# Kernel optimization log

Hardware: AMD Instinct MI355X
Metric: run time of the kernel (lower is better)

Reference implementation:

```python
import jax, jax.numpy as jnp
import numpy as np
from jax import lax

B, T, D = 1, 2048, 2048
H, KVH, HD = 16, 4, 128
BETA = 0.9
ROPE_BASE = 10000.0


def _causal_prefix_ema(x, beta):
    # x: (B, T, D); m_t = beta * m_{t-1} + (1 - beta) * x_t, m_{-1} = 0
    def step(m, xt):
        m = beta * m + (1.0 - beta) * xt
        return m, m
    _, ys = lax.scan(step, jnp.zeros_like(x[:, 0]), jnp.swapaxes(x, 0, 1))
    return jnp.swapaxes(ys, 0, 1)


def _rotate_half(x):
    x1, x2 = jnp.split(x, 2, axis=-1)
    return jnp.concatenate([-x2, x1], axis=-1)


def _rope_cos_sin(t, hd, dtype):
    inv_freq = 1.0 / (ROPE_BASE ** (jnp.arange(0, hd, 2, dtype=jnp.float32) / hd))
    freqs = jnp.arange(t, dtype=jnp.float32)[:, None] * inv_freq[None, :]  # (T, HD/2)
    emb = jnp.concatenate([freqs, freqs], axis=-1)  # (T, HD)
    return jnp.cos(emb).astype(dtype)[None, None], jnp.sin(emb).astype(dtype)[None, None]


def setup_inputs() -> dict:
    key = jax.random.key(0)
    ks = jax.random.split(key, 8)
    std = 0.02
    return {
        "hidden_states": jax.random.normal(ks[0], (B, T, D), jnp.float32),
        "Wq": jax.random.normal(ks[1], (D, H * HD), jnp.float32) * std,
        "Wk": jax.random.normal(ks[2], (D, KVH * HD), jnp.float32) * std,
        "Wv": jax.random.normal(ks[3], (D, KVH * HD), jnp.float32) * std,
        "Wo": jax.random.normal(ks[4], (H * HD, D), jnp.float32) * std,
        "Wr1": jax.random.normal(ks[5], (D, D // 2), jnp.float32) * std,
        "br1": jnp.zeros((D // 2,), jnp.float32),
        "Wr2": jax.random.normal(ks[6], (D // 2, 2), jnp.float32) * std,
        "br2": jnp.zeros((2,), jnp.float32),
    }


def reference(hidden_states, Wq, Wk, Wv, Wo, Wr1, br1, Wr2, br2):
    b, t, d = hidden_states.shape
    q = hidden_states @ Wq  # (B, T, H*HD)

    # multi-level memories: l1 = raw, l2 = causal prefix EMA
    l2 = _causal_prefix_ema(hidden_states, BETA)

    # router MLP on q + softmax over levels
    h = jax.nn.silu(q @ Wr1 + br1)
    lam = jax.nn.softmax(h @ Wr2 + br2, axis=-1)  # (B, T, 2)
    fused = lam[..., 0:1] * hidden_states + lam[..., 1:2] * l2

    # shape to heads
    q_s = q.reshape(b, t, H, HD).transpose(0, 2, 1, 3)                 # (B, H, T, HD)
    k_s = (fused @ Wk).reshape(b, t, KVH, HD).transpose(0, 2, 1, 3)    # (B, KVH, T, HD)
    v_s = (fused @ Wv).reshape(b, t, KVH, HD).transpose(0, 2, 1, 3)

    # RoPE
    cos, sin = _rope_cos_sin(t, HD, q_s.dtype)
    q_s = q_s * cos + _rotate_half(q_s) * sin
    k_s = k_s * cos + _rotate_half(k_s) * sin

    # repeat kv for GQA
    n_rep = H // KVH
    k_s = jnp.repeat(k_s, n_rep, axis=1)
    v_s = jnp.repeat(v_s, n_rep, axis=1)

    # causal SDPA
    scale = 1.0 / jnp.sqrt(jnp.asarray(HD, q_s.dtype))
    scores = jnp.einsum("bhqd,bhkd->bhqk", q_s, k_s) * scale
    causal = jnp.tril(jnp.ones((t, t), dtype=bool))
    scores = jnp.where(causal[None, None], scores, jnp.finfo(scores.dtype).min)
    attn = jax.nn.softmax(scores, axis=-1)
    out = jnp.einsum("bhqk,bhkd->bhqd", attn, v_s)  # (B, H, T, HD)

    out = out.transpose(0, 2, 1, 3).reshape(b, t, H * HD)
    return out @ Wo
```

## Files before the change

### kernel.cpp

```cpp
#include <hip/hip_runtime.h>
#include <hip/hip_bf16.h>

#define T_SEQ 2048
#define D_MODEL 2048
#define NH 16
#define NKVH 4
#define HD 128

typedef __attribute__((ext_vector_type(8))) short bf16x8;
typedef __attribute__((ext_vector_type(4))) float f32x4;

static __device__ __forceinline__ short f32_to_bf16(float f) {
    unsigned u = __float_as_uint(f);
    u += 0x7fffu + ((u >> 16) & 1u);
    return (short)(u >> 16);
}
static __device__ __forceinline__ float bf16_to_f32(short s) {
    return __uint_as_float(((unsigned)(unsigned short)s) << 16);
}
static __device__ __forceinline__ void gl_to_lds16(const void* g, void* l) {
    __builtin_amdgcn_global_load_lds(
        (const __attribute__((address_space(1))) unsigned int*)g,
        (__attribute__((address_space(3))) unsigned int*)l, 16, 0, 0);
}

template<int BN>
__global__ __launch_bounds__(256, 2) void gemm_bt_kernel(
    const short* __restrict__ A, const short* __restrict__ Bt,
    float* __restrict__ Cf, short* __restrict__ Cb,
    int M, int N, int K, const float* __restrict__ bias, int act)
{
    constexpr int NI = BN / 64;
    constexpr int BCH = BN / 32;
    __shared__ short Alds[2][64 * 64];
    __shared__ short Blds[2][BN * 64];

    const int tid = threadIdx.x;
    const int wave = tid >> 6, lane = tid & 63;
    const int l16 = lane & 15, quad = lane >> 4;
    const int wn = wave * (BN / 4);
    const int m0 = blockIdx.y * 64, n0 = blockIdx.x * BN;
    const int niter = K >> 6;

    f32x4 acc[4][NI] = {};

    #pragma unroll
    for (int p = 0; p < 2; ++p) {
        int li = p * 256 + tid;
        int row = li >> 3, sc = li & 7;
        gl_to_lds16(A + (size_t)(m0 + row) * K + ((sc ^ (row & 7)) * 8),
                    &Alds[0][(size_t)(p * 256 + wave * 64) * 8]);
    }
    #pragma unroll
    for (int p = 0; p < BCH; ++p) {
        int li = p * 256 + tid;
        int row = li >> 3, sc = li & 7;
        gl_to_lds16(Bt + (size_t)(n0 + row) * K + ((sc ^ (row & 7)) * 8),
                    &Blds[0][(size_t)(p * 256 + wave * 64) * 8]);
    }

    for (int t = 0; t < niter; ++t) {
        asm volatile("s_waitcnt vmcnt(0)\n\ts_barrier" ::: "memory");

        if (t + 1 < niter) {
            int k1 = (t + 1) << 6;
            int nb = (t + 1) & 1;
            #pragma unroll
            for (int p = 0; p < 2; ++p) {
                int li = p * 256 + tid;
                int row = li >> 3, sc = li & 7;
                gl_to_lds16(A + (size_t)(m0 + row) * K + k1 + ((sc ^ (row & 7)) * 8),
                            &Alds[nb][(size_t)(p * 256 + wave * 64) * 8]);
            }
            #pragma unroll
            for (int p = 0; p < BCH; ++p) {
                int li = p * 256 + tid;
                int row = li >> 3, sc = li & 7;
                gl_to_lds16(Bt + (size_t)(n0 + row) * K + k1 + ((sc ^ (row & 7)) * 8),
                            &Blds[nb][(size_t)(p * 256 + wave * 64) * 8]);
            }
        }

        const short* Ab = Alds[t & 1];
        const short* Bb = Blds[t & 1];
        #pragma unroll
        for (int kk = 0; kk < 2; ++kk) {
            bf16x8 a[4], b[NI];
            #pragma unroll
            for (int i = 0; i < 4; ++i)
                a[i] = *(const bf16x8*)
                    &Ab[(size_t)(i * 16 + l16) * 64 + (((kk * 4 + quad) ^ (l16 & 7)) * 8)];
            #pragma unroll
            for (int i = 0; i < NI; ++i)
                b[i] = *(const bf16x8*)
                    &Bb[(size_t)(wn + i * 16 + l16) * 64 + (((kk * 4 + quad) ^ (l16 & 7)) * 8)];
            #pragma unroll
            for (int mi = 0; mi < 4; ++mi)
                #pragma unroll
                for (int ni = 0; ni < NI; ++ni)
                    acc[mi][ni] = __builtin_amdgcn_mfma_f32_16x16x32_bf16(
                        a[mi], b[ni], acc[mi][ni], 0, 0, 0);
        }
    }

    #pragma unroll
    for (int mi = 0; mi < 4; ++mi) {
        #pragma unroll
        for (int ni = 0; ni < NI; ++ni) {
            int col = n0 + wn + ni * 16 + l16;
            float bv = bias ? bias[col] : 0.0f;
            #pragma unroll
            for (int r = 0; r < 4; ++r) {
                int row = m0 + mi * 16 + quad * 4 + r;
                float x = acc[mi][ni][r] + bv;
                if (act) x = x / (1.0f + __expf(-x));
                size_t o = (size_t)row * N + col;
                if (Cf) Cf[o] = x;
                if (Cb) Cb[o] = f32_to_bf16(x);
            }
        }
    }
}

__global__ __launch_bounds__(256) void transpose_all_kernel(
    const float* __restrict__ Wq, const float* __restrict__ Wk,
    const float* __restrict__ Wv, const float* __restrict__ Wr1,
    const float* __restrict__ Wo, short* __restrict__ Wq_t,
    short* __restrict__ Wkv_t, short* __restrict__ Wr1_t,
    short* __restrict__ Wo_t)
{
    __shared__ float tile[32][33];
    int bx = blockIdx.x;
    const float* src; short* dst; int ld, cb;
    if (bx < 64)       { src = Wq;  dst = Wq_t;  ld = 2048; cb = bx; }
    else if (bx < 80)  { src = Wk;  dst = Wkv_t; ld = 512;  cb = bx - 64; }
    else if (bx < 96)  { src = Wv;  dst = Wkv_t + (size_t)512 * 2048; ld = 512; cb = bx - 80; }
    else if (bx < 128) { src = Wr1; dst = Wr1_t; ld = 1024; cb = bx - 96; }
    else               { src = Wo;  dst = Wo_t;  ld = 2048; cb = bx - 128; }
    int c0 = cb * 32, r0 = blockIdx.y * 32;
    int t = threadIdx.x;
    int r = t >> 3, c4 = (t & 7) * 4;
    float4 v = *(const float4*)&src[(size_t)(r0 + r) * ld + c0 + c4];
    tile[r][c4 + 0] = v.x; tile[r][c4 + 1] = v.y;
    tile[r][c4 + 2] = v.z; tile[r][c4 + 3] = v.w;
    __syncthreads();
    short o[4];
    #pragma unroll
    for (int j = 0; j < 4; ++j) o[j] = f32_to_bf16(tile[c4 + j][r]);
    *(uint2*)&dst[(size_t)(c0 + r) * 2048 + r0 + c4] = *(const uint2*)o;
}

__global__ __launch_bounds__(256) void transpose_bf_kernel(
    const short* __restrict__ src, int ld, short* __restrict__ dst, int ldd)
{
    __shared__ float tile[32][33];
    int r0 = blockIdx.y * 32, c0 = blockIdx.x * 32;
    int x = threadIdx.x & 31, y = threadIdx.x >> 5;
    #pragma unroll
    for (int i = 0; i < 4; ++i)
        tile[y + i * 8][x] = bf16_to_f32(src[(size_t)(r0 + y + i * 8) * ld + c0 + x]);
    __syncthreads();
    #pragma unroll
    for (int i = 0; i < 4; ++i)
        dst[(size_t)(c0 + y + i * 8) * ldd + r0 + x] = f32_to_bf16(tile[x][y + i * 8]);
}

__global__ __launch_bounds__(256) void ema_kernel(const float* __restrict__ hs,
                                                  float* __restrict__ l2,
                                                  short* __restrict__ hs_b)
{
    int d = blockIdx.y * 256 + threadIdx.x;
    int t0 = blockIdx.x * 128;
    int ts = t0 - 192; if (ts < 0) ts = 0;
    float m = 0.0f;
    for (int tb = ts; tb < t0; tb += 16) {
        float buf[16];
        #pragma unroll
        for (int j = 0; j < 16; ++j) buf[j] = hs[(size_t)(tb + j) * D_MODEL + d];
        #pragma unroll
        for (int j = 0; j < 16; ++j) m = 0.9f * m + 0.1f * buf[j];
    }
    for (int tb = t0; tb < t0 + 128; tb += 16) {
        float buf[16];
        #pragma unroll
        for (int j = 0; j < 16; ++j) buf[j] = hs[(size_t)(tb + j) * D_MODEL + d];
        #pragma unroll
        for (int j = 0; j < 16; ++j) hs_b[(size_t)(tb + j) * D_MODEL + d] = f32_to_bf16(buf[j]);
        #pragma unroll
        for (int j = 0; j < 16; ++j) { m = 0.9f * m + 0.1f * buf[j]; buf[j] = m; }
        #pragma unroll
        for (int j = 0; j < 16; ++j) l2[(size_t)(tb + j) * D_MODEL + d] = buf[j];
    }
}

__global__ __launch_bounds__(64) void lam_kernel(
    const short* __restrict__ h, const float* __restrict__ Wr2,
    const float* __restrict__ br2, float* __restrict__ lam)
{
    int t = blockIdx.x;
    int lane = threadIdx.x;
    float z0 = 0.0f, z1 = 0.0f;
    for (int i = lane; i < 1024; i += 64) {
        float hv = bf16_to_f32(h[(size_t)t * 1024 + i]);
        z0 += hv * Wr2[i * 2 + 0];
        z1 += hv * Wr2[i * 2 + 1];
    }
    #pragma unroll
    for (int off = 1; off < 64; off <<= 1) {
        z0 += __shfl_xor(z0, off);
        z1 += __shfl_xor(z1, off);
    }
    if (lane == 0) {
        z0 += br2[0]; z1 += br2[1];
        float mx = fmaxf(z0, z1);
        float e0 = expf(z0 - mx), e1 = expf(z1 - mx);
        float inv = 1.0f / (e0 + e1);
        lam[t * 2 + 0] = e0 * inv;
        lam[t * 2 + 1] = e1 * inv;
    }
}

__global__ void fuse_kernel(const float* __restrict__ hs, const float* __restrict__ l2,
                            const float* __restrict__ lam, short* __restrict__ fused)
{
    int idx = blockIdx.x * blockDim.x + threadIdx.x;
    int t = idx >> 9;
    float a0 = lam[t * 2 + 0], a1 = lam[t * 2 + 1];
    float4 a = ((const float4*)hs)[idx];
    float4 b = ((const float4*)l2)[idx];
    short o[4] = {f32_to_bf16(a0 * a.x + a1 * b.x), f32_to_bf16(a0 * a.y + a1 * b.y),
                  f32_to_bf16(a0 * a.z + a1 * b.z), f32_to_bf16(a0 * a.w + a1 * b.w)};
    *(uint2*)(fused + (size_t)idx * 4) = *(const uint2*)o;
}

__global__ void rope_q_kernel(const short* __restrict__ q, short* __restrict__ qr)
{
    int idx = blockIdx.x * blockDim.x + threadIdx.x;
    int d = idx & 63;
    int h = (idx >> 6) & 15;
    int t = idx >> 10;
    float fr = (float)t * __expf(-(float)d * 0.14391156831212787f);
    float s, c;
    sincosf(fr, &s, &c);
    const float sc = 0.08838834764831845f;
    const short* src = q + (size_t)t * D_MODEL + h * HD;
    float x1 = bf16_to_f32(src[d]) * sc, x2 = bf16_to_f32(src[d + 64]) * sc;
    short* dst = qr + ((size_t)h * T_SEQ + t) * HD;
    dst[d]      = f32_to_bf16(x1 * c - x2 * s);
    dst[d + 64] = f32_to_bf16(x2 * c + x1 * s);
}

__global__ void rope_k_kernel(const short* __restrict__ kv, short* __restrict__ kr)
{
    int idx = blockIdx.x * blockDim.x + threadIdx.x;
    int d = idx & 63;
    int kh = (idx >> 6) & 3;
    int t = idx >> 8;
    float fr = (float)t * __expf(-(float)d * 0.14391156831212787f);
    float s, c;
    sincosf(fr, &s, &c);
    const short* src = kv + (size_t)t * 1024 + kh * HD;
    float x1 = bf16_to_f32(src[d]), x2 = bf16_to_f32(src[d + 64]);
    short* dst = kr + ((size_t)kh * T_SEQ + t) * HD;
    dst[d]      = f32_to_bf16(x1 * c - x2 * s);
    dst[d + 64] = f32_to_bf16(x2 * c + x1 * s);
}

__global__ __launch_bounds__(256, 1) void attn_kernel(
    const short* __restrict__ Qr, const short* __restrict__ Kr,
    const short* __restrict__ Vt, short* __restrict__ Out)
{
    const int h = blockIdx.x;
    const int qt = blockIdx.y;
    const int kvh = h >> 2;
    const int tid = threadIdx.x;
    const int wave = tid >> 6, lane = tid & 63;
    const int l16 = lane & 15, quad = lane >> 4;

    __shared__ short Klds[2][128 * 128];
    __shared__ short Vlds[2][128 * 128];
    __shared__ short Plds[4][32][128];

    const short* kbase = Kr + (size_t)kvh * T_SEQ * HD;
    const short* vbase = Vt + (size_t)kvh * HD * T_SEQ;

    const int qbase = qt * 128 + wave * 32;
    const int n = qt + 1;

    bf16x8 qf[2][4];
    #pragma unroll
    for (int m = 0; m < 2; ++m) {
        const short* qrow = Qr + ((size_t)h * T_SEQ + qbase + m * 16 + l16) * HD;
        #pragma unroll
        for (int kc = 0; kc < 4; ++kc)
            qf[m][kc] = *(const bf16x8*)&qrow[kc * 32 + quad * 8];
    }
    f32x4 o[2][8] = {};
    float lsum[2][4] = {};

    {
        #pragma unroll
        for (int p = 0; p < 8; ++p) {
            int li = p * 256 + tid;
            int row = li >> 4, gs = (li & 15) ^ (row & 15);
            gl_to_lds16(kbase + (size_t)row * HD + gs * 8,
                        &Klds[0][(size_t)(p * 256 + wave * 64) * 8]);
        }
        #pragma unroll
        for (int p = 0; p < 8; ++p) {
            int li = p * 256 + tid;
            int row = li >> 4, gs = (li & 15) ^ (row & 15);
            gl_to_lds16(vbase + (size_t)row * T_SEQ + gs * 8,
                        &Vlds[0][(size_t)(p * 256 + wave * 64) * 8]);
        }
    }

    for (int t = 0; t < n; ++t) {
        asm volatile("s_waitcnt vmcnt(0)\n\ts_barrier" ::: "memory");

        if (t + 1 < n) {
            int kv1 = (t + 1) << 7;
            int nb = (t + 1) & 1;
            const short* ks = kbase + (size_t)kv1 * HD;
            #pragma unroll
            for (int p = 0; p < 8; ++p) {
                int li = p * 256 + tid;
                int row = li >> 4, gs = (li & 15) ^ (row & 15);
                gl_to_lds16(ks + (size_t)row * HD + gs * 8,
                            &Klds[nb][(size_t)(p * 256 + wave * 64) * 8]);
            }
            #pragma unroll
            for (int p = 0; p < 8; ++p) {
                int li = p * 256 + tid;
                int row = li >> 4, gs = (li & 15) ^ (row & 15);
                gl_to_lds16(vbase + (size_t)row * T_SEQ + kv1 + gs * 8,
                            &Vlds[nb][(size_t)(p * 256 + wave * 64) * 8]);
            }
        }

        const short* Kb = Klds[t & 1];
        const short* Vb = Vlds[t & 1];

        f32x4 s[2][8];
        #pragma unroll
        for (int m = 0; m < 2; ++m)
            #pragma unroll
            for (int ni = 0; ni < 8; ++ni) s[m][ni] = (f32x4){0, 0, 0, 0};
        __builtin_amdgcn_s_setprio(1);
        #pragma unroll
        for (int ni = 0; ni < 8; ++ni)
            #pragma unroll
            for (int kc = 0; kc < 4; ++kc) {
                bf16x8 b = *(const bf16x8*)
                    &Kb[(size_t)(ni * 16 + l16) * 128 + (((kc * 4 + quad) ^ l16) * 8)];
                s[0][ni] = __builtin_amdgcn_mfma_f32_16x16x32_bf16(qf[0][kc], b, s[0][ni], 0, 0, 0);
                s[1][ni] = __builtin_amdgcn_mfma_f32_16x16x32_bf16(qf[1][kc], b, s[1][ni], 0, 0, 0);
            }
        __builtin_amdgcn_s_setprio(0);

        if (t == n - 1) {
            int kvg0 = t << 7;
            #pragma unroll
            for (int m = 0; m < 2; ++m)
                #pragma unroll
                for (int ni = 0; ni < 8; ++ni) {
                    int kvg = kvg0 + ni * 16 + l16;
                    #pragma unroll
                    for (int r = 0; r < 4; ++r) {
                        int qg = qbase + m * 16 + quad * 4 + r;
                        float p = (kvg <= qg) ? __expf(s[m][ni][r]) : 0.0f;
                        lsum[m][r] += p;
                        int prow = quad * 4 + r, pcol = ni * 16 + l16;
                        Plds[wave][m * 16 + prow][(((pcol >> 3) ^ prow) * 8) + (pcol & 7)] =
                            f32_to_bf16(p);
                    }
                }
        } else {
            #pragma unroll
            for (int m = 0; m < 2; ++m)
                #pragma unroll
                for (int ni = 0; ni < 8; ++ni)
                    #pragma unroll
                    for (int r = 0; r < 4; ++r) {
                        float p = __expf(s[m][ni][r]);
                        lsum[m][r] += p;
                        int prow = quad * 4 + r, pcol = ni * 16 + l16;
                        Plds[wave][m * 16 + prow][(((pcol >> 3) ^ prow) * 8) + (pcol & 7)] =
                            f32_to_bf16(p);
                    }
        }
        asm volatile("s_waitcnt lgkmcnt(0)" ::: "memory");

        __builtin_amdgcn_s_setprio(1);
        #pragma unroll
        for (int kc = 0; kc < 4; ++kc) {
            bf16x8 pa0 = *(const bf16x8*)
                &Plds[wave][l16][(((kc * 4 + quad) ^ l16) * 8)];
            bf16x8 pa1 = *(const bf16x8*)
                &Plds[wave][16 + l16][(((kc * 4 + quad) ^ l16) * 8)];
            #pragma unroll
            for (int d8 = 0; d8 < 8; ++d8) {
                bf16x8 b = *(const bf16x8*)
                    &Vb[(size_t)(d8 * 16 + l16) * 128 + (((kc * 4 + quad) ^ l16) * 8)];
                o[0][d8] = __builtin_amdgcn_mfma_f32_16x16x32_bf16(pa0, b, o[0][d8], 0, 0, 0);
                o[1][d8] = __builtin_amdgcn_mfma_f32_16x16x32_bf16(pa1, b, o[1][d8], 0, 0, 0);
            }
        }
        __builtin_amdgcn_s_setprio(0);
    }

    #pragma unroll
    for (int m = 0; m < 2; ++m)
        #pragma unroll
        for (int r = 0; r < 4; ++r) {
            #pragma unroll
            for (int off = 1; off < 16; off <<= 1)
                lsum[m][r] += __shfl_xor(lsum[m][r], off);
            lsum[m][r] = 1.0f / lsum[m][r];
        }
    #pragma unroll
    for (int m = 0; m < 2; ++m)
        #pragma unroll
        for (int d8 = 0; d8 < 8; ++d8)
            #pragma unroll
            for (int r = 0; r < 4; ++r) {
                int row = qbase + m * 16 + quad * 4 + r;
                Out[(size_t)row * D_MODEL + h * HD + d8 * 16 + l16] =
                    f32_to_bf16(o[m][d8][r] * lsum[m][r]);
            }
}

extern "C" void kernel_launch(void* const* d_in, const int* in_sizes, int n_in,
                              void* d_out, int out_size, void* d_ws, size_t ws_size,
                              hipStream_t stream)
{
    const float* hs  = (const float*)d_in[0];
    const float* Wq  = (const float*)d_in[1];
    const float* Wk  = (const float*)d_in[2];
    const float* Wv  = (const float*)d_in[3];
    const float* Wo  = (const float*)d_in[4];
    const float* Wr1 = (const float*)d_in[5];
    const float* br1 = (const float*)d_in[6];
    const float* Wr2 = (const float*)d_in[7];
    const float* br2 = (const float*)d_in[8];
    float* out = (float*)d_out;

    char* w = (char*)d_ws;
    const size_t MB = 1u << 20;
    float* l2_f     = (float*)(w + 0 * MB);
    short* hs_bf    = (short*)(w + 16 * MB);
    short* Wq_t     = (short*)(w + 24 * MB);
    short* Wkv_t    = (short*)(w + 32 * MB);
    short* Wr1_t    = (short*)(w + 36 * MB);
    short* Wo_t     = (short*)(w + 40 * MB);
    short* q_bf     = (short*)(w + 48 * MB);
    short* h_bf     = (short*)(w + 56 * MB);
    short* fused_bf = (short*)(w + 60 * MB);
    short* kv_bf    = (short*)(w + 68 * MB);
    short* qr       = (short*)(w + 72 * MB);
    short* kr       = (short*)(w + 80 * MB);
    short* vr       = (short*)(w + 82 * MB);
    float* lam_f    = (float*)(w + 84 * MB);
    short* attn_bf  = hs_bf;

    transpose_all_kernel<<<dim3(192, 64), 256, 0, stream>>>(
        Wq, Wk, Wv, Wr1, Wo, Wq_t, Wkv_t, Wr1_t, Wo_t);

    ema_kernel<<<dim3(T_SEQ / 128, D_MODEL / 256), 256, 0, stream>>>(hs, l2_f, hs_bf);

    gemm_bt_kernel<128><<<dim3(16, 32), 256, 0, stream>>>(
        hs_bf, Wq_t, nullptr, q_bf, 2048, 2048, 2048, nullptr, 0);

    gemm_bt_kernel<64><<<dim3(16, 32), 256, 0, stream>>>(
        q_bf, Wr1_t, nullptr, h_bf, 2048, 1024, 2048, br1, 1);

    lam_kernel<<<T_SEQ, 64, 0, stream>>>(h_bf, Wr2, br2, lam_f);

    fuse_kernel<<<(T_SEQ * D_MODEL / 4) / 256, 256, 0, stream>>>(hs, l2_f, lam_f, fused_bf);

    gemm_bt_kernel<64><<<dim3(16, 32), 256, 0, stream>>>(
        fused_bf, Wkv_t, nullptr, kv_bf, 2048, 1024, 2048, nullptr, 0);

    rope_q_kernel<<<(T_SEQ * NH * 64) / 256, 256, 0, stream>>>(q_bf, qr);
    rope_k_kernel<<<(T_SEQ * NKVH * 64) / 256, 256, 0, stream>>>(kv_bf, kr);
    transpose_bf_kernel<<<dim3(16, 64), 256, 0, stream>>>(kv_bf + 512, 1024, vr, 2048);

    attn_kernel<<<dim3(NH, 16), 256, 0, stream>>>(qr, kr, vr, attn_bf);

    gemm_bt_kernel<128><<<dim3(16, 32), 256, 0, stream>>>(
        attn_bf, Wo_t, out, nullptr, 2048, 2048, 2048, nullptr, 0);
}
```

Measured before the change: 350.1 us.

## Split attention KV tile across two wave groups with LDS reduction

The attention kernel now runs 512 threads per block: two groups of four waves each handle one half (64 keys) of every 128-key tile for the same query rows. The partial outputs and row sums are combined through shared memory at the end. This doubles the waves available to hide latency in a grid of only 256 blocks, since the attention grid underfills the GPU. The cost is a 160KB LDS footprint, an extra reduction pass with two barriers, and fewer MFMAs per wave per tile.

```diff
diff --git a/kernel.cpp b/kernel.cpp
--- a/kernel.cpp
+++ b/kernel.cpp
@@ -266,7 +266,7 @@
     dst[d + 64] = f32_to_bf16(x2 * c + x1 * s);
 }
 
-__global__ __launch_bounds__(256, 1) void attn_kernel(
+__global__ __launch_bounds__(512, 2) void attn_kernel(
     const short* __restrict__ Qr, const short* __restrict__ Kr,
     const short* __restrict__ Vt, short* __restrict__ Out)
 {
@@ -276,15 +276,19 @@
     const int tid = threadIdx.x;
     const int wave = tid >> 6, lane = tid & 63;
     const int l16 = lane & 15, quad = lane >> 4;
-
-    __shared__ short Klds[2][128 * 128];
-    __shared__ short Vlds[2][128 * 128];
-    __shared__ short Plds[4][32][128];
+    const int wq = wave & 3;
+    const int wk = wave >> 2;
+
+    __shared__ __align__(16) char smem[163840];
+    short* Klds = (short*)smem;
+    short* Vlds = (short*)(smem + 65536);
+    short* Plds = (short*)(smem + 131072);
 
     const short* kbase = Kr + (size_t)kvh * T_SEQ * HD;
     const short* vbase = Vt + (size_t)kvh * HD * T_SEQ;
 
-    const int qbase = qt * 128 + wave * 32;
+    const int qbase = qt * 128 + wq * 32;
+    const int ko = wk * 64;
     const int n = qt + 1;
 
     bf16x8 qf[2][4];
@@ -300,18 +304,18 @@
 
     {
         #pragma unroll
-        for (int p = 0; p < 8; ++p) {
-            int li = p * 256 + tid;
+        for (int p = 0; p < 4; ++p) {
+            int li = p * 512 + tid;
             int row = li >> 4, gs = (li & 15) ^ (row & 15);
             gl_to_lds16(kbase + (size_t)row * HD + gs * 8,
-                        &Klds[0][(size_t)(p * 256 + wave * 64) * 8]);
-        }
-        #pragma unroll
-        for (int p = 0; p < 8; ++p) {
-            int li = p * 256 + tid;
+                        &Klds[(size_t)(p * 512 + wave * 64) * 8]);
+        }
+        #pragma unroll
+        for (int p = 0; p < 4; ++p) {
+            int li = p * 512 + tid;
             int row = li >> 4, gs = (li & 15) ^ (row & 15);
             gl_to_lds16(vbase + (size_t)row * T_SEQ + gs * 8,
-                        &Vlds[0][(size_t)(p * 256 + wave * 64) * 8]);
+                        &Vlds[(size_t)(p * 512 + wave * 64) * 8]);
         }
     }
 
@@ -323,47 +327,47 @@
             int nb = (t + 1) & 1;
             const short* ks = kbase + (size_t)kv1 * HD;
             #pragma unroll
-            for (int p = 0; p < 8; ++p) {
-                int li = p * 256 + tid;
+            for (int p = 0; p < 4; ++p) {
+                int li = p * 512 + tid;
                 int row = li >> 4, gs = (li & 15) ^ (row & 15);
                 gl_to_lds16(ks + (size_t)row * HD + gs * 8,
-                            &Klds[nb][(size_t)(p * 256 + wave * 64) * 8]);
-            }
-            #pragma unroll
-            for (int p = 0; p < 8; ++p) {
-                int li = p * 256 + tid;
+                            &Klds[(size_t)(nb * 16384 + (p * 512 + wave * 64) * 8)]);
+            }
+            #pragma unroll
+            for (int p = 0; p < 4; ++p) {
+                int li = p * 512 + tid;
                 int row = li >> 4, gs = (li & 15) ^ (row & 15);
                 gl_to_lds16(vbase + (size_t)row * T_SEQ + kv1 + gs * 8,
-                            &Vlds[nb][(size_t)(p * 256 + wave * 64) * 8]);
-            }
-        }
-
-        const short* Kb = Klds[t & 1];
-        const short* Vb = Vlds[t & 1];
-
-        f32x4 s[2][8];
+                            &Vlds[(size_t)(nb * 16384 + (p * 512 + wave * 64) * 8)]);
+            }
+        }
+
+        const short* Kb = Klds + (size_t)(t & 1) * 16384;
+        const short* Vb = Vlds + (size_t)(t & 1) * 16384;
+
+        f32x4 s[2][4];
         #pragma unroll
         for (int m = 0; m < 2; ++m)
             #pragma unroll
-            for (int ni = 0; ni < 8; ++ni) s[m][ni] = (f32x4){0, 0, 0, 0};
+            for (int ni = 0; ni < 4; ++ni) s[m][ni] = (f32x4){0, 0, 0, 0};
         __builtin_amdgcn_s_setprio(1);
         #pragma unroll
-        for (int ni = 0; ni < 8; ++ni)
+        for (int ni = 0; ni < 4; ++ni)
             #pragma unroll
             for (int kc = 0; kc < 4; ++kc) {
                 bf16x8 b = *(const bf16x8*)
-                    &Kb[(size_t)(ni * 16 + l16) * 128 + (((kc * 4 + quad) ^ l16) * 8)];
+                    &Kb[(size_t)(ko + ni * 16 + l16) * 128 + (((kc * 4 + quad) ^ l16) * 8)];
                 s[0][ni] = __builtin_amdgcn_mfma_f32_16x16x32_bf16(qf[0][kc], b, s[0][ni], 0, 0, 0);
                 s[1][ni] = __builtin_amdgcn_mfma_f32_16x16x32_bf16(qf[1][kc], b, s[1][ni], 0, 0, 0);
             }
         __builtin_amdgcn_s_setprio(0);
 
         if (t == n - 1) {
-            int kvg0 = t << 7;
+            int kvg0 = (t << 7) + ko;
             #pragma unroll
             for (int m = 0; m < 2; ++m)
                 #pragma unroll
-                for (int ni = 0; ni < 8; ++ni) {
+                for (int ni = 0; ni < 4; ++ni) {
                     int kvg = kvg0 + ni * 16 + l16;
                     #pragma unroll
                     for (int r = 0; r < 4; ++r) {
@@ -371,37 +375,38 @@
                         float p = (kvg <= qg) ? __expf(s[m][ni][r]) : 0.0f;
                         lsum[m][r] += p;
                         int prow = quad * 4 + r, pcol = ni * 16 + l16;
-                        Plds[wave][m * 16 + prow][(((pcol >> 3) ^ prow) * 8) + (pcol & 7)] =
-                            f32_to_bf16(p);
+                        Plds[wave * 2048 + (m * 16 + prow) * 64 +
+                             (((pcol >> 3) ^ (prow & 7)) * 8) + (pcol & 7)] = f32_to_bf16(p);
                     }
                 }
         } else {
             #pragma unroll
             for (int m = 0; m < 2; ++m)
                 #pragma unroll
-                for (int ni = 0; ni < 8; ++ni)
+                for (int ni = 0; ni < 4; ++ni)
                     #pragma unroll
                     for (int r = 0; r < 4; ++r) {
                         float p = __expf(s[m][ni][r]);
                         lsum[m][r] += p;
                         int prow = quad * 4 + r, pcol = ni * 16 + l16;
-                        Plds[wave][m * 16 + prow][(((pcol >> 3) ^ prow) * 8) + (pcol & 7)] =
-                            f32_to_bf16(p);
+                        Plds[wave * 2048 + (m * 16 + prow) * 64 +
+                             (((pcol >> 3) ^ (prow & 7)) * 8) + (pcol & 7)] = f32_to_bf16(p);
                     }
         }
         asm volatile("s_waitcnt lgkmcnt(0)" ::: "memory");
 
         __builtin_amdgcn_s_setprio(1);
         #pragma unroll
-        for (int kc = 0; kc < 4; ++kc) {
+        for (int kc = 0; kc < 2; ++kc) {
             bf16x8 pa0 = *(const bf16x8*)
-                &Plds[wave][l16][(((kc * 4 + quad) ^ l16) * 8)];
+                &Plds[wave * 2048 + l16 * 64 + (((kc * 4 + quad) ^ (l16 & 7)) * 8)];
             bf16x8 pa1 = *(const bf16x8*)
-                &Plds[wave][16 + l16][(((kc * 4 + quad) ^ l16) * 8)];
+                &Plds[wave * 2048 + (16 + l16) * 64 + (((kc * 4 + quad) ^ (l16 & 7)) * 8)];
             #pragma unroll
             for (int d8 = 0; d8 < 8; ++d8) {
                 bf16x8 b = *(const bf16x8*)
-                    &Vb[(size_t)(d8 * 16 + l16) * 128 + (((kc * 4 + quad) ^ l16) * 8)];
+                    &Vb[(size_t)(d8 * 16 + l16) * 128 +
+                        (((wk * 8 + kc * 4 + quad) ^ l16) * 8)];
                 o[0][d8] = __builtin_amdgcn_mfma_f32_16x16x32_bf16(pa0, b, o[0][d8], 0, 0, 0);
                 o[1][d8] = __builtin_amdgcn_mfma_f32_16x16x32_bf16(pa1, b, o[1][d8], 0, 0, 0);
             }
@@ -409,25 +414,53 @@
         __builtin_amdgcn_s_setprio(0);
     }
 
-    #pragma unroll
-    for (int m = 0; m < 2; ++m)
-        #pragma unroll
-        for (int r = 0; r < 4; ++r) {
-            #pragma unroll
-            for (int off = 1; off < 16; off <<= 1)
-                lsum[m][r] += __shfl_xor(lsum[m][r], off);
-            lsum[m][r] = 1.0f / lsum[m][r];
-        }
-    #pragma unroll
-    for (int m = 0; m < 2; ++m)
-        #pragma unroll
-        for (int d8 = 0; d8 < 8; ++d8)
+    __syncthreads();
+    float* Ox = (float*)smem;
+    float* Lx = (float*)(smem + 67584);
+    if (wk) {
+        #pragma unroll
+        for (int m = 0; m < 2; ++m)
+            #pragma unroll
+            for (int d8 = 0; d8 < 8; ++d8)
+                #pragma unroll
+                for (int r = 0; r < 4; ++r)
+                    Ox[(wq * 32 + m * 16 + quad * 4 + r) * 132 + d8 * 16 + l16] = o[m][d8][r];
+        #pragma unroll
+        for (int m = 0; m < 2; ++m)
+            #pragma unroll
+            for (int r = 0; r < 4; ++r)
+                Lx[(wq * 32 + m * 16 + quad * 4 + r) * 16 + l16] = lsum[m][r];
+    }
+    __syncthreads();
+    if (!wk) {
+        #pragma unroll
+        for (int m = 0; m < 2; ++m)
+            #pragma unroll
+            for (int d8 = 0; d8 < 8; ++d8)
+                #pragma unroll
+                for (int r = 0; r < 4; ++r)
+                    o[m][d8][r] += Ox[(wq * 32 + m * 16 + quad * 4 + r) * 132 + d8 * 16 + l16];
+        #pragma unroll
+        for (int m = 0; m < 2; ++m)
             #pragma unroll
             for (int r = 0; r < 4; ++r) {
-                int row = qbase + m * 16 + quad * 4 + r;
-                Out[(size_t)row * D_MODEL + h * HD + d8 * 16 + l16] =
-                    f32_to_bf16(o[m][d8][r] * lsum[m][r]);
-            }
+                lsum[m][r] += Lx[(wq * 32 + m * 16 + quad * 4 + r) * 16 + l16];
+                #pragma unroll
+                for (int off = 1; off < 16; off <<= 1)
+                    lsum[m][r] += __shfl_xor(lsum[m][r], off);
+                lsum[m][r] = 1.0f / lsum[m][r];
+            }
+        #pragma unroll
+        for (int m = 0; m < 2; ++m)
+            #pragma unroll
+            for (int d8 = 0; d8 < 8; ++d8)
+                #pragma unroll
+                for (int r = 0; r < 4; ++r) {
+                    int row = qbase + m * 16 + quad * 4 + r;
+                    Out[(size_t)row * D_MODEL + h * HD + d8 * 16 + l16] =
+                        f32_to_bf16(o[m][d8][r] * lsum[m][r]);
+                }
+    }
 }
 
 extern "C" void kernel_launch(void* const* d_in, const int* in_sizes, int n_in,
@@ -485,7 +518,7 @@
     rope_k_kernel<<<(T_SEQ * NKVH * 64) / 256, 256, 0, stream>>>(kv_bf, kr);
     transpose_bf_kernel<<<dim3(16, 64), 256, 0, stream>>>(kv_bf + 512, 1024, vr, 2048);
 
-    attn_kernel<<<dim3(NH, 16), 256, 0, stream>>>(qr, kr, vr, attn_bf);
+    attn_kernel<<<dim3(NH, 16), 512, 0, stream>>>(qr, kr, vr, attn_bf);
 
     gemm_bt_kernel<128><<<dim3(16, 32), 256, 0, stream>>>(
         attn_bf, Wo_t, out, nullptr, 2048, 2048, 2048, nullptr, 0);
```

New measurement: 321.6 us. -8.1%, faster.
